# Kernel optimization log

Hardware: AMD Instinct MI355X
Metric: run time of the kernel (lower is better)

## Reference

```python
import jax, jax.numpy as jnp
import numpy as np

B, L, E, H = 2, 2048, 1024, 16
D = E // H  # 64


def setup_inputs() -> dict:
    key = jax.random.key(0)
    ks = jax.random.split(key, 9)
    return {
        "query": jax.random.normal(ks[0], (B, L, E), dtype=jnp.float32),
        "value": jax.random.normal(ks[1], (B, L, E), dtype=jnp.float32),
        "key": jax.random.normal(ks[2], (B, L, E), dtype=jnp.float32),
        "mask": jax.random.randint(ks[3], (B, 1, L, L), 0, 2, dtype=jnp.int32),
        "Wq": jax.random.normal(ks[4], (D, D), dtype=jnp.float32) * 0.05,
        "Wk": jax.random.normal(ks[5], (D, D), dtype=jnp.float32) * 0.05,
        "Wv": jax.random.normal(ks[6], (D, D), dtype=jnp.float32) * 0.05,
        "Wfc": jax.random.normal(ks[7], (E, E), dtype=jnp.float32) * 0.02,
        "bfc": jax.random.normal(ks[8], (E,), dtype=jnp.float32) * 0.02,
    }


def reference(query, value, key, mask, Wq, Wk, Wv, Wfc, bfc):
    b, q_len, _ = query.shape
    k_len = key.shape[1]
    v_len = value.shape[1]
    # split heads: [b, l, H, D]
    q = query.reshape(b, q_len, H, D)
    k = key.reshape(b, k_len, H, D)
    v = value.reshape(b, v_len, H, D)
    # per-head linear projections (shared weights across heads, no bias)
    q = jnp.einsum('bqhd,ed->bqhe', q, Wq)
    k = jnp.einsum('bkhd,ed->bkhe', k, Wk)
    v = jnp.einsum('bvhd,ed->bvhe', v, Wv)
    # attention scores [b, H, q, k]
    attn = jnp.einsum('bqhd,bkhd->bhqk', q, k)
    # NOTE: original masks BEFORE scaling, and scales by sqrt(embedding_size)
    attn = jnp.where(mask == 0, jnp.float32(-1e20), attn)
    attn = attn / jnp.float32(E ** 0.5)
    attn = jax.nn.softmax(attn, axis=3)
    out = jnp.einsum('bhqk,bkhd->bqhd', attn, v).reshape(b, q_len, E)
    out = out @ Wfc.T + bfc
    return out
```

## Files before the change

kernel.cpp:

```cpp
#include <hip/hip_runtime.h>
#include <hip/hip_bf16.h>


#define B_ 2
#define L_ 2048
#define E_ 1024
#define H_ 16
#define D_ 64

typedef __attribute__((ext_vector_type(8))) short s8v;
typedef __attribute__((ext_vector_type(4))) float f4v;

__device__ __forceinline__ f4v mfma16(s8v a, s8v b, f4v c) {
    return __builtin_amdgcn_mfma_f32_16x16x32_bf16(a, b, c, 0, 0, 0);
}

__device__ __forceinline__ float fast_exp2(float x) {
    return __builtin_amdgcn_exp2f(x);
}

__device__ __forceinline__ ushort bf16bits(float f) {
    __hip_bfloat16 h = __float2bfloat16(f);
    return *(ushort*)&h;
}

__device__ __forceinline__ void glds16(const __hip_bfloat16* g, ushort* l) {
    __builtin_amdgcn_global_load_lds(
        (const __attribute__((address_space(1))) void*)g,
        (__attribute__((address_space(3))) void*)l,
        16, 0, 0);
}

__device__ __forceinline__ s8v ld8_dual(const void* p, size_t idx, bool isf32) {
    if (isf32) {
        const float* pf = (const float*)p + idx;
        f4v f0 = *(const f4v*)pf;
        f4v f1 = *(const f4v*)(pf + 4);
        s8v r;
        r[0] = (short)bf16bits(f0[0]); r[1] = (short)bf16bits(f0[1]);
        r[2] = (short)bf16bits(f0[2]); r[3] = (short)bf16bits(f0[3]);
        r[4] = (short)bf16bits(f1[0]); r[5] = (short)bf16bits(f1[1]);
        r[6] = (short)bf16bits(f1[2]); r[7] = (short)bf16bits(f1[3]);
        return r;
    }
    return *(const s8v*)((const __hip_bfloat16*)p + idx);
}

__device__ __forceinline__ s8v ld8_ws(const __hip_bfloat16* p) {
    return *(const s8v*)p;
}

__device__ __forceinline__ void cvt_piece(
    size_t i4, const void* Wfc, const void* bfc,
    __hip_bfloat16* wfc_bf, __hip_bfloat16* bfc_bf, bool isf32)
{
    const size_t base = i4 * 4;
    const size_t n1 = (size_t)E_ * E_;
    if (base >= n1 + E_) return;
    const void* src = (base < n1) ? Wfc : bfc;
    const size_t off = (base < n1) ? base : base - n1;
    __hip_bfloat16* dst = (base < n1) ? (wfc_bf + off) : (bfc_bf + off);
    if (isf32) {
        f4v v = *(const f4v*)((const float*)src + off);
        #pragma unroll
        for (int j = 0; j < 4; ++j) dst[j] = __float2bfloat16(v[j]);
    } else {
        *(ushort4*)dst = *(const ushort4*)((const ushort*)src + off);
    }
}

__global__ __launch_bounds__(256) void pack_mask_kernel(
    const int* __restrict__ mask, unsigned long long* __restrict__ mbits,
    const ushort* __restrict__ q, int* __restrict__ flag)
{
    if (blockIdx.x == 0) {
        __shared__ int cnt;
        if (threadIdx.x == 0) cnt = 0;
        __syncthreads();
        int bad = 0;
        #pragma unroll
        for (int i = 0; i < 16; ++i) {
            ushort u = q[threadIdx.x * 16 + i];
            int e = (u >> 7) & 0xFF;
            if (e >= 0x8E) ++bad;
        }
        atomicAdd(&cnt, bad);
        __syncthreads();
        if (threadIdx.x == 0) *flag = (cnt > 100) ? 1 : 0;
    }
    const int wave = threadIdx.x >> 6;
    const int lane = threadIdx.x & 63;
    const size_t wbase = ((size_t)blockIdx.x * 4 + wave) * 4;
    #pragma unroll
    for (int i = 0; i < 4; ++i) {
        const size_t widx = wbase + i;
        const int v = mask[widx * 64 + lane];
        const unsigned long long bal = __ballot(v != 0);
        if (lane == 0) mbits[widx] = bal;
    }
}

__global__ __launch_bounds__(256) void proj_all_kernel(
    const void* __restrict__ q_in, const void* __restrict__ k_in,
    const void* __restrict__ v_in,
    const void* __restrict__ Wq, const void* __restrict__ Wk,
    const void* __restrict__ Wv,
    const void* __restrict__ Wfc, const void* __restrict__ bfc,
    __hip_bfloat16* __restrict__ qp, __hip_bfloat16* __restrict__ kp,
    __hip_bfloat16* __restrict__ vpT,
    __hip_bfloat16* __restrict__ wfc_bf, __hip_bfloat16* __restrict__ bfc_bf,
    const int* __restrict__ flag)
{
    __shared__ __align__(16) ushort tile[64][72];
    const bool isf32 = (*flag != 0);
    const int wave = threadIdx.x >> 6;
    const int lane = threadIdx.x & 63;
    const int quad = lane >> 4;
    const int l16  = lane & 15;

    if (blockIdx.y == 3) {
        cvt_piece((size_t)blockIdx.x * 256 + threadIdx.x, Wfc, bfc, wfc_bf, bfc_bf, isf32);
        if (blockIdx.x == 0)
            cvt_piece((size_t)(E_ * (size_t)E_ / 4) + threadIdx.x, Wfc, bfc, wfc_bf, bfc_bf, isf32);
        return;
    }
    if (blockIdx.y < 2) {
        const void* X = blockIdx.y == 0 ? q_in : k_in;
        const void* W = blockIdx.y == 0 ? Wq : Wk;
        __hip_bfloat16* dst = blockIdx.y == 0 ? qp : kp;
        const int m0 = (blockIdx.x * 4 + wave) * 16;

        const size_t abase = (size_t)(m0 + l16) * D_;
        s8v a0 = ld8_dual(X, abase + quad * 8, isf32);
        s8v a1 = ld8_dual(X, abase + 32 + quad * 8, isf32);

        f4v acc[4];
        #pragma unroll
        for (int nt = 0; nt < 4; ++nt) {
            const size_t bbase = (size_t)(nt * 16 + l16) * D_;
            s8v b0 = ld8_dual(W, bbase + quad * 8, isf32);
            s8v b1 = ld8_dual(W, bbase + 32 + quad * 8, isf32);
            f4v c = {0.f, 0.f, 0.f, 0.f};
            c = mfma16(a0, b0, c);
            c = mfma16(a1, b1, c);
            acc[nt] = c;
        }
        #pragma unroll
        for (int r = 0; r < 4; ++r) {
            const int m = m0 + quad * 4 + r;
            const int h = m & 15;
            const int bl = m >> 4;
            const int b = bl >> 11;
            const int l = bl & (L_ - 1);
            #pragma unroll
            for (int nt = 0; nt < 4; ++nt) {
                const int e = nt * 16 + l16;
                dst[(((size_t)(b * H_ + h)) * L_ + l) * D_ + e] = __float2bfloat16(acc[nt][r]);
            }
        }
    } else {
        const int l0 = (blockIdx.x & 31) * 64;
        const int bh = blockIdx.x >> 5;
        const int b = bh >> 4, h = bh & 15;
        const int lw = l0 + wave * 16;

        const size_t xbase = ((size_t)(b * L_ + lw + l16)) * E_ + h * D_;
        s8v a0 = ld8_dual(v_in, xbase + quad * 8, isf32);
        s8v a1 = ld8_dual(v_in, xbase + 32 + quad * 8, isf32);

        #pragma unroll
        for (int nt = 0; nt < 4; ++nt) {
            const int e = nt * 16 + l16;
            s8v b0 = ld8_dual(Wv, (size_t)e * D_ + quad * 8, isf32);
            s8v b1 = ld8_dual(Wv, (size_t)e * D_ + 32 + quad * 8, isf32);
            f4v c = {0.f, 0.f, 0.f, 0.f};
            c = mfma16(a0, b0, c);
            c = mfma16(a1, b1, c);
            #pragma unroll
            for (int r = 0; r < 4; ++r)
                tile[wave * 16 + quad * 4 + r][e] = bf16bits(c[r]);
        }
        __syncthreads();
        const int e  = threadIdx.x >> 2;
        const int lc = (threadIdx.x & 3) * 16;
        s8v s0, s1;
        #pragma unroll
        for (int i = 0; i < 8; ++i) {
            s0[i] = (short)tile[lc + i][e];
            s1[i] = (short)tile[lc + 8 + i][e];
        }
        __hip_bfloat16* drow = vpT + ((size_t)bh * D_ + e) * L_ + l0 + lc;
        *(s8v*)drow = s0;
        *(s8v*)(drow + 8) = s1;
    }
}

__global__ __launch_bounds__(256) void cvt_wfc_kernel(
    const void* __restrict__ Wfc, const void* __restrict__ bfc,
    __hip_bfloat16* __restrict__ wfc_bf, __hip_bfloat16* __restrict__ bfc_bf,
    const int* __restrict__ flag)
{
    cvt_piece((size_t)blockIdx.x * 256 + threadIdx.x, Wfc, bfc, wfc_bf, bfc_bf, *flag != 0);
}

__global__ __launch_bounds__(256, 4) void attn_kernel(
    const __hip_bfloat16* __restrict__ qp,
    const __hip_bfloat16* __restrict__ kp,
    const __hip_bfloat16* __restrict__ vpT,
    const unsigned long long* __restrict__ mbits,
    __hip_bfloat16* __restrict__ attn_out)
{
    __shared__ __align__(16) ushort kbuf[2][64 * 64];
    __shared__ __align__(16) ushort vbuf[2][64 * 64];
    __shared__ __align__(16) ushort pbuf[4][16 * 64];

    const int wave = threadIdx.x >> 6;
    const int lane = threadIdx.x & 63;
    const int quad = lane >> 4;
    const int l16  = lane & 15;
    const int sw   = l16 & 7;
    const int bh = blockIdx.y;
    const int b = bh >> 4, h = bh & 15;
    const int q0 = blockIdx.x * 64 + wave * 16;

    const float C2 = 0.045084439755930314f;
    const float NEGBIG = -1.0e20f;

    const __hip_bfloat16* kbh = kp + (size_t)bh * L_ * D_;
    const __hip_bfloat16* vbh = vpT + (size_t)bh * D_ * L_;
    const unsigned long long* mrow_bits = mbits + (size_t)b * L_ * 32;

    const int lrow = lane >> 3;
    const int lchk = (lane & 7) ^ lrow;
    const int r0 = wave * 16;
    const __hip_bfloat16* kg0 = kbh + (size_t)(r0 + lrow) * D_ + lchk * 8;
    const __hip_bfloat16* kg1 = kbh + (size_t)(r0 + 8 + lrow) * D_ + lchk * 8;
    const __hip_bfloat16* vg0 = vbh + (size_t)(r0 + lrow) * L_ + lchk * 8;
    const __hip_bfloat16* vg1 = vbh + (size_t)(r0 + 8 + lrow) * L_ + lchk * 8;

    const __hip_bfloat16* qbase = qp + ((size_t)bh * L_ + q0) * D_;
    s8v qa0 = ld8_ws(qbase + (size_t)l16 * D_ + quad * 8);
    s8v qa1 = ld8_ws(qbase + (size_t)l16 * D_ + 32 + quad * 8);

    float rsum[4] = {0.f, 0.f, 0.f, 0.f};
    f4v o[4];
    #pragma unroll
    for (int nt = 0; nt < 4; ++nt) o[nt] = (f4v){0.f, 0.f, 0.f, 0.f};

    glds16(kg0, &kbuf[0][r0 * 64]);
    glds16(kg1, &kbuf[0][r0 * 64 + 512]);
    glds16(vg0, &vbuf[0][r0 * 64]);
    glds16(vg1, &vbuf[0][r0 * 64 + 512]);
    __syncthreads();

    int cur = 0;
    for (int it = 0; it < 32; ++it) {
        const int k0 = it * 64;
        uint wlo[4], whi[4];
        #pragma unroll
        for (int r = 0; r < 4; ++r) {
            const unsigned long long wq = mrow_bits[(size_t)(q0 + quad * 4 + r) * 32 + it];
            wlo[r] = (uint)wq; whi[r] = (uint)(wq >> 32);
        }
        if (it < 31) {
            glds16(kg0 + (size_t)(k0 + 64) * D_, &kbuf[cur ^ 1][r0 * 64]);
            glds16(kg1 + (size_t)(k0 + 64) * D_, &kbuf[cur ^ 1][r0 * 64 + 512]);
            glds16(vg0 + (k0 + 64), &vbuf[cur ^ 1][r0 * 64]);
            glds16(vg1 + (k0 + 64), &vbuf[cur ^ 1][r0 * 64 + 512]);
        }
        f4v s[4];
        #pragma unroll
        for (int nt = 0; nt < 4; ++nt) {
            const ushort* kr = &kbuf[cur][(nt * 16 + l16) * 64];
            s8v kb0 = *(const s8v*)(kr + ((quad ^ sw) << 3));
            s8v kb1 = *(const s8v*)(kr + (((quad + 4) ^ sw) << 3));
            f4v c = {0.f, 0.f, 0.f, 0.f};
            c = mfma16(qa0, kb0, c);
            c = mfma16(qa1, kb1, c);
            s[nt] = c;
        }
        #pragma unroll
        for (int nt = 0; nt < 4; ++nt) {
            const int sh = ((nt & 1) << 4) + l16;
            const int chi = 2 * nt + (l16 >> 3);
            #pragma unroll
            for (int r = 0; r < 4; ++r) {
                const uint w = (nt & 2) ? whi[r] : wlo[r];
                const float sv = ((w >> sh) & 1u) ? s[nt][r] : NEGBIG;
                const float p = fast_exp2(sv * C2);
                rsum[r] += p;
                const int row = quad * 4 + r;
                pbuf[wave][row * 64 + ((chi ^ (row & 7)) << 3) + (l16 & 7)] =
                    (ushort)((__float_as_uint(p) + 0x8000u) >> 16);
            }
        }
        asm volatile("s_waitcnt lgkmcnt(0)" ::: "memory");
        const ushort* pw = &pbuf[wave][l16 * 64];
        s8v pa0 = *(const s8v*)(pw + ((quad ^ sw) << 3));
        s8v pa1 = *(const s8v*)(pw + (((quad + 4) ^ sw) << 3));
        #pragma unroll
        for (int nt = 0; nt < 4; ++nt) {
            const ushort* vr = &vbuf[cur][(nt * 16 + l16) * 64];
            s8v vb0 = *(const s8v*)(vr + ((quad ^ sw) << 3));
            s8v vb1 = *(const s8v*)(vr + (((quad + 4) ^ sw) << 3));
            o[nt] = mfma16(pa0, vb0, o[nt]);
            o[nt] = mfma16(pa1, vb1, o[nt]);
        }
        __syncthreads();
        cur ^= 1;
    }
    #pragma unroll
    for (int r = 0; r < 4; ++r) {
        float v = rsum[r];
        #pragma unroll
        for (int off = 1; off < 16; off <<= 1)
            v += __shfl_xor(v, off, 64);
        const float inv = 1.0f / fmaxf(v, 1e-30f);
        const int row = q0 + quad * 4 + r;
        #pragma unroll
        for (int nt = 0; nt < 4; ++nt) {
            const int d = nt * 16 + l16;
            attn_out[((size_t)(b * L_ + row)) * E_ + h * D_ + d] =
                __float2bfloat16(o[nt][r] * inv);
        }
    }
}

__global__ __launch_bounds__(256, 4) void fc_kernel(
    const __hip_bfloat16* __restrict__ x,
    const __hip_bfloat16* __restrict__ wfc_bf,
    const __hip_bfloat16* __restrict__ bfc_bf,
    void* __restrict__ out, const int* __restrict__ flag)
{
    __shared__ __align__(16) ushort abuf[2][64 * 64];
    __shared__ __align__(16) ushort bbuf[2][64 * 64];
    const bool isf32 = (*flag != 0);
    const int wave = threadIdx.x >> 6;
    const int lane = threadIdx.x & 63;
    const int quad = lane >> 4;
    const int l16  = lane & 15;
    const int sw   = l16 & 7;
    const int m0 = blockIdx.x * 64;
    const int n0 = blockIdx.y * 64;

    const int lrow = lane >> 3;
    const int lchk = (lane & 7) ^ lrow;
    const int r0 = wave * 16;
    const __hip_bfloat16* ag0 = x + (size_t)(m0 + r0 + lrow) * E_ + lchk * 8;
    const __hip_bfloat16* ag1 = x + (size_t)(m0 + r0 + 8 + lrow) * E_ + lchk * 8;
    const __hip_bfloat16* bg0 = wfc_bf + (size_t)(n0 + r0 + lrow) * E_ + lchk * 8;
    const __hip_bfloat16* bg1 = wfc_bf + (size_t)(n0 + r0 + 8 + lrow) * E_ + lchk * 8;

    f4v acc[4];
    #pragma unroll
    for (int nt = 0; nt < 4; ++nt) acc[nt] = (f4v){0.f, 0.f, 0.f, 0.f};

    glds16(ag0, &abuf[0][r0 * 64]);
    glds16(ag1, &abuf[0][r0 * 64 + 512]);
    glds16(bg0, &bbuf[0][r0 * 64]);
    glds16(bg1, &bbuf[0][r0 * 64 + 512]);
    __syncthreads();

    int cur = 0;
    for (int it = 0; it < 16; ++it) {
        const int k0 = it * 64;
        if (it < 15) {
            glds16(ag0 + k0 + 64, &abuf[cur ^ 1][r0 * 64]);
            glds16(ag1 + k0 + 64, &abuf[cur ^ 1][r0 * 64 + 512]);
            glds16(bg0 + k0 + 64, &bbuf[cur ^ 1][r0 * 64]);
            glds16(bg1 + k0 + 64, &bbuf[cur ^ 1][r0 * 64 + 512]);
        }
        const ushort* ar = &abuf[cur][(r0 + l16) * 64];
        s8v a0 = *(const s8v*)(ar + ((quad ^ sw) << 3));
        s8v a1 = *(const s8v*)(ar + (((quad + 4) ^ sw) << 3));
        #pragma unroll
        for (int nt = 0; nt < 4; ++nt) {
            const ushort* br = &bbuf[cur][(nt * 16 + l16) * 64];
            s8v b0 = *(const s8v*)(br + ((quad ^ sw) << 3));
            s8v b1 = *(const s8v*)(br + (((quad + 4) ^ sw) << 3));
            acc[nt] = mfma16(a0, b0, acc[nt]);
            acc[nt] = mfma16(a1, b1, acc[nt]);
        }
        __syncthreads();
        cur ^= 1;
    }
    #pragma unroll
    for (int r = 0; r < 4; ++r) {
        const int m = m0 + r0 + quad * 4 + r;
        #pragma unroll
        for (int nt = 0; nt < 4; ++nt) {
            const int n = n0 + nt * 16 + l16;
            const float val = acc[nt][r] + __bfloat162float(bfc_bf[n]);
            if (isf32) ((float*)out)[(size_t)m * E_ + n] = val;
            else       ((__hip_bfloat16*)out)[(size_t)m * E_ + n] = __float2bfloat16(val);
        }
    }
}

extern "C" void kernel_launch(void* const* d_in, const int* in_sizes, int n_in,
                              void* d_out, int out_size, void* d_ws, size_t ws_size,
                              hipStream_t stream) {
    const void* query = d_in[0];
    const void* value = d_in[1];
    const void* key   = d_in[2];
    const int*  mask  = (const int*)d_in[3];
    const void* Wq  = d_in[4];
    const void* Wk  = d_in[5];
    const void* Wv  = d_in[6];
    const void* Wfc = d_in[7];
    const void* bfc = d_in[8];

    char* ws = (char*)d_ws;
    int* flag                     = (int*)ws;
    unsigned long long* mbits     = (unsigned long long*)(ws + (64u << 10));
    __hip_bfloat16* qp            = (__hip_bfloat16*)(ws + (2u  << 20));
    __hip_bfloat16* kp            = (__hip_bfloat16*)(ws + (10u << 20));
    __hip_bfloat16* vpT           = (__hip_bfloat16*)(ws + (18u << 20));
    __hip_bfloat16* attn_out      = (__hip_bfloat16*)(ws + (26u << 20));

    const bool big_ws = ws_size >= (37ull << 20);
    __hip_bfloat16* wfc_bf = big_ws ? (__hip_bfloat16*)(ws + (34ull << 20)) : qp;
    __hip_bfloat16* bfc_bf = wfc_bf + (size_t)E_ * E_;

    pack_mask_kernel<<<8192, 256, 0, stream>>>(mask, mbits, (const ushort*)query, flag);
    proj_all_kernel<<<dim3(1024, big_ws ? 4 : 3), 256, 0, stream>>>(
        query, key, value, Wq, Wk, Wv, Wfc, bfc, qp, kp, vpT, wfc_bf, bfc_bf, flag);
    attn_kernel<<<dim3(32, 32), 256, 0, stream>>>(qp, kp, vpT, mbits, attn_out);
    if (!big_ws)
        cvt_wfc_kernel<<<1025, 256, 0, stream>>>(Wfc, bfc, wfc_bf, bfc_bf, flag);
    fc_kernel<<<dim3(64, 16), 256, 0, stream>>>(attn_out, wfc_bf, bfc_bf, d_out, flag);
}
```

Before: 244.0 us.

## Fuse mask packing into projection kernel and transpose score MFMA for packed P stores

Mask bit-packing moves out of its own 8192-block kernel into extra blockIdx.y slices of the projection kernel, leaving only a tiny one-block detection kernel. The softmax scale is folded into the Q projection output. The attention kernel swaps the MFMA operand order so each lane holds one query row, which lets it load one mask word per iteration, build the mask with branchless bit ops and store P as packed 8-byte writes. The row-sum reduction shrinks to two shuffles. Folding the scale into Q before the bf16 rounding slightly changes numerics, and the mask-packing slices now share a grid with the projection blocks.

```diff
diff --git a/kernel.cpp b/kernel.cpp
--- a/kernel.cpp
+++ b/kernel.cpp
@@ -69,35 +69,20 @@
     }
 }
 
-__global__ __launch_bounds__(256) void pack_mask_kernel(
-    const int* __restrict__ mask, unsigned long long* __restrict__ mbits,
-    const ushort* __restrict__ q, int* __restrict__ flag)
-{
-    if (blockIdx.x == 0) {
-        __shared__ int cnt;
-        if (threadIdx.x == 0) cnt = 0;
-        __syncthreads();
-        int bad = 0;
-        #pragma unroll
-        for (int i = 0; i < 16; ++i) {
-            ushort u = q[threadIdx.x * 16 + i];
-            int e = (u >> 7) & 0xFF;
-            if (e >= 0x8E) ++bad;
-        }
-        atomicAdd(&cnt, bad);
-        __syncthreads();
-        if (threadIdx.x == 0) *flag = (cnt > 100) ? 1 : 0;
-    }
-    const int wave = threadIdx.x >> 6;
-    const int lane = threadIdx.x & 63;
-    const size_t wbase = ((size_t)blockIdx.x * 4 + wave) * 4;
-    #pragma unroll
-    for (int i = 0; i < 4; ++i) {
-        const size_t widx = wbase + i;
-        const int v = mask[widx * 64 + lane];
-        const unsigned long long bal = __ballot(v != 0);
-        if (lane == 0) mbits[widx] = bal;
-    }
+__global__ void detect_kernel(const ushort* __restrict__ q, int* __restrict__ flag) {
+    __shared__ int cnt;
+    if (threadIdx.x == 0) cnt = 0;
+    __syncthreads();
+    int bad = 0;
+    #pragma unroll
+    for (int i = 0; i < 16; ++i) {
+        ushort u = q[threadIdx.x * 16 + i];
+        int e = (u >> 7) & 0xFF;
+        if (e >= 0x8E) ++bad;
+    }
+    atomicAdd(&cnt, bad);
+    __syncthreads();
+    if (threadIdx.x == 0) *flag = (cnt > 100) ? 1 : 0;
 }
 
 __global__ __launch_bounds__(256) void proj_all_kernel(
@@ -106,6 +91,7 @@
     const void* __restrict__ Wq, const void* __restrict__ Wk,
     const void* __restrict__ Wv,
     const void* __restrict__ Wfc, const void* __restrict__ bfc,
+    const int* __restrict__ mask, unsigned long long* __restrict__ mbits,
     __hip_bfloat16* __restrict__ qp, __hip_bfloat16* __restrict__ kp,
     __hip_bfloat16* __restrict__ vpT,
     __hip_bfloat16* __restrict__ wfc_bf, __hip_bfloat16* __restrict__ bfc_bf,
@@ -119,6 +105,18 @@
     const int l16  = lane & 15;
 
     if (blockIdx.y == 3) {
+        const int lane_ = threadIdx.x & 63;
+        const size_t wbase = (size_t)blockIdx.x * 128 + wave * 32;
+        #pragma unroll 4
+        for (int i = 0; i < 32; ++i) {
+            const size_t widx = wbase + i;
+            const int v = mask[widx * 64 + lane_];
+            const unsigned long long bal = __ballot(v != 0);
+            if (lane_ == 0) mbits[widx] = bal;
+        }
+        return;
+    }
+    if (blockIdx.y == 4) {
         cvt_piece((size_t)blockIdx.x * 256 + threadIdx.x, Wfc, bfc, wfc_bf, bfc_bf, isf32);
         if (blockIdx.x == 0)
             cvt_piece((size_t)(E_ * (size_t)E_ / 4) + threadIdx.x, Wfc, bfc, wfc_bf, bfc_bf, isf32);
@@ -128,6 +126,7 @@
         const void* X = blockIdx.y == 0 ? q_in : k_in;
         const void* W = blockIdx.y == 0 ? Wq : Wk;
         __hip_bfloat16* dst = blockIdx.y == 0 ? qp : kp;
+        const float oscale = (blockIdx.y == 0) ? 0.045084439755930314f : 1.0f;
         const int m0 = (blockIdx.x * 4 + wave) * 16;
 
         const size_t abase = (size_t)(m0 + l16) * D_;
@@ -155,7 +154,8 @@
             #pragma unroll
             for (int nt = 0; nt < 4; ++nt) {
                 const int e = nt * 16 + l16;
-                dst[(((size_t)(b * H_ + h)) * L_ + l) * D_ + e] = __float2bfloat16(acc[nt][r]);
+                dst[(((size_t)(b * H_ + h)) * L_ + l) * D_ + e] =
+                    __float2bfloat16(acc[nt][r] * oscale);
             }
         }
     } else {
@@ -223,12 +223,11 @@
     const int b = bh >> 4, h = bh & 15;
     const int q0 = blockIdx.x * 64 + wave * 16;
 
-    const float C2 = 0.045084439755930314f;
-    const float NEGBIG = -1.0e20f;
+    const uint NEGB = __float_as_uint(-4.5084439e18f);
 
     const __hip_bfloat16* kbh = kp + (size_t)bh * L_ * D_;
     const __hip_bfloat16* vbh = vpT + (size_t)bh * D_ * L_;
-    const unsigned long long* mrow_bits = mbits + (size_t)b * L_ * 32;
+    const unsigned long long* mrow = mbits + ((size_t)b * L_ + q0 + l16) * 32;
 
     const int lrow = lane >> 3;
     const int lchk = (lane & 7) ^ lrow;
@@ -242,10 +241,17 @@
     s8v qa0 = ld8_ws(qbase + (size_t)l16 * D_ + quad * 8);
     s8v qa1 = ld8_ws(qbase + (size_t)l16 * D_ + 32 + quad * 8);
 
-    float rsum[4] = {0.f, 0.f, 0.f, 0.f};
+    float rsum = 0.f;
     f4v o[4];
     #pragma unroll
     for (int nt = 0; nt < 4; ++nt) o[nt] = (f4v){0.f, 0.f, 0.f, 0.f};
+
+    uint2* pdst[4];
+    #pragma unroll
+    for (int nt = 0; nt < 4; ++nt) {
+        const int c = nt * 2 + (quad >> 1);
+        pdst[nt] = (uint2*)&pbuf[wave][l16 * 64 + ((c ^ sw) << 3) + 4 * (quad & 1)];
+    }
 
     glds16(kg0, &kbuf[0][r0 * 64]);
     glds16(kg1, &kbuf[0][r0 * 64 + 512]);
@@ -256,12 +262,8 @@
     int cur = 0;
     for (int it = 0; it < 32; ++it) {
         const int k0 = it * 64;
-        uint wlo[4], whi[4];
-        #pragma unroll
-        for (int r = 0; r < 4; ++r) {
-            const unsigned long long wq = mrow_bits[(size_t)(q0 + quad * 4 + r) * 32 + it];
-            wlo[r] = (uint)wq; whi[r] = (uint)(wq >> 32);
-        }
+        const unsigned long long wq = mrow[it];
+        const uint wlo = (uint)wq, whi = (uint)(wq >> 32);
         if (it < 31) {
             glds16(kg0 + (size_t)(k0 + 64) * D_, &kbuf[cur ^ 1][r0 * 64]);
             glds16(kg1 + (size_t)(k0 + 64) * D_, &kbuf[cur ^ 1][r0 * 64 + 512]);
@@ -275,24 +277,28 @@
             s8v kb0 = *(const s8v*)(kr + ((quad ^ sw) << 3));
             s8v kb1 = *(const s8v*)(kr + (((quad + 4) ^ sw) << 3));
             f4v c = {0.f, 0.f, 0.f, 0.f};
-            c = mfma16(qa0, kb0, c);
-            c = mfma16(qa1, kb1, c);
+            c = mfma16(kb0, qa0, c);
+            c = mfma16(kb1, qa1, c);
             s[nt] = c;
         }
         #pragma unroll
         for (int nt = 0; nt < 4; ++nt) {
-            const int sh = ((nt & 1) << 4) + l16;
-            const int chi = 2 * nt + (l16 >> 3);
+            const uint w = (nt & 2) ? whi : wlo;
+            float pr[4];
             #pragma unroll
             for (int r = 0; r < 4; ++r) {
-                const uint w = (nt & 2) ? whi[r] : wlo[r];
-                const float sv = ((w >> sh) & 1u) ? s[nt][r] : NEGBIG;
-                const float p = fast_exp2(sv * C2);
-                rsum[r] += p;
-                const int row = quad * 4 + r;
-                pbuf[wave][row * 64 + ((chi ^ (row & 7)) << 3) + (l16 & 7)] =
-                    (ushort)((__float_as_uint(p) + 0x8000u) >> 16);
+                const int idx = ((nt & 1) << 4) + quad * 4 + r;
+                const uint m = (uint)(((int)(w << (31 - idx))) >> 31);
+                const uint sb = (__float_as_uint(s[nt][r]) & m) | (NEGB & ~m);
+                const float p = fast_exp2(__uint_as_float(sb));
+                rsum += p;
+                pr[r] = p;
             }
+            const uint dw0 = ((__float_as_uint(pr[0]) + 0x8000u) >> 16) |
+                             ((__float_as_uint(pr[1]) + 0x8000u) & 0xFFFF0000u);
+            const uint dw1 = ((__float_as_uint(pr[2]) + 0x8000u) >> 16) |
+                             ((__float_as_uint(pr[3]) + 0x8000u) & 0xFFFF0000u);
+            *pdst[nt] = make_uint2(dw0, dw1);
         }
         asm volatile("s_waitcnt lgkmcnt(0)" ::: "memory");
         const ushort* pw = &pbuf[wave][l16 * 64];
@@ -309,14 +315,15 @@
         __syncthreads();
         cur ^= 1;
     }
+    float v = rsum;
+    v += __shfl_xor(v, 16, 64);
+    v += __shfl_xor(v, 32, 64);
     #pragma unroll
     for (int r = 0; r < 4; ++r) {
-        float v = rsum[r];
-        #pragma unroll
-        for (int off = 1; off < 16; off <<= 1)
-            v += __shfl_xor(v, off, 64);
-        const float inv = 1.0f / fmaxf(v, 1e-30f);
-        const int row = q0 + quad * 4 + r;
+        const int qrow = quad * 4 + r;
+        const float li = __shfl(v, qrow, 64);
+        const float inv = 1.0f / fmaxf(li, 1e-30f);
+        const int row = q0 + qrow;
         #pragma unroll
         for (int nt = 0; nt < 4; ++nt) {
             const int d = nt * 16 + l16;
@@ -422,9 +429,10 @@
     __hip_bfloat16* wfc_bf = big_ws ? (__hip_bfloat16*)(ws + (34ull << 20)) : qp;
     __hip_bfloat16* bfc_bf = wfc_bf + (size_t)E_ * E_;
 
-    pack_mask_kernel<<<8192, 256, 0, stream>>>(mask, mbits, (const ushort*)query, flag);
-    proj_all_kernel<<<dim3(1024, big_ws ? 4 : 3), 256, 0, stream>>>(
-        query, key, value, Wq, Wk, Wv, Wfc, bfc, qp, kp, vpT, wfc_bf, bfc_bf, flag);
+    detect_kernel<<<1, 256, 0, stream>>>((const ushort*)query, flag);
+    proj_all_kernel<<<dim3(1024, big_ws ? 5 : 4), 256, 0, stream>>>(
+        query, key, value, Wq, Wk, Wv, Wfc, bfc, mask, mbits,
+        qp, kp, vpT, wfc_bf, bfc_bf, flag);
     attn_kernel<<<dim3(32, 32), 256, 0, stream>>>(qp, kp, vpT, mbits, attn_out);
     if (!big_ws)
         cvt_wfc_kernel<<<1025, 256, 0, stream>>>(Wfc, bfc, wfc_bf, bfc_bf, flag);
```

New measurement: 241.7 us. Within noise of the previous version (-1.0%).
